# Kernel optimization log

Hardware: AMD Instinct MI355X
Metric: run time of the kernel (lower is better)

## Reference

```python
import jax, jax.numpy as jnp
import numpy as np

BS, NS, NM, NO = 262144, 16, 8, 8

def setup_inputs() -> dict:
    key = jax.random.key(0)
    k = jax.random.split(key, 6)
    z = jax.random.normal(k[0], (BS, NM), dtype=jnp.float32)
    x0 = jax.random.normal(k[1], (BS, NS), dtype=jnp.float32)
    A = jax.random.normal(k[2], (BS, NS, NS), dtype=jnp.float32) * 0.1
    # PSD initial covariance per batch element
    P0 = jnp.einsum('bij,bkj->bik', A, A) + jnp.eye(NS, dtype=jnp.float32)
    phi = jnp.eye(NS, dtype=jnp.float32) + 0.01 * jax.random.normal(k[3], (NS, NS), dtype=jnp.float32)
    H = jax.random.normal(k[4], (NM, NS), dtype=jnp.float32) * 0.3
    C = jax.random.normal(k[5], (NO, NS), dtype=jnp.float32) * 0.3
    Qdiag = jnp.full((NS,), 0.1, dtype=jnp.float32)
    Rdiag = jnp.full((NM,), 0.1, dtype=jnp.float32)
    return {"z": z, "x0": x0, "P0": P0, "phi": phi, "H": H, "C": C,
            "Qdiag": Qdiag, "Rdiag": Rdiag}

def reference(z, x0, P0, phi, H, C, Qdiag, Rdiag):
    # --- predict ---
    x_pred = x0 @ phi.T                                       # [bs, ns]
    P_pred = jnp.einsum('ij,bjk,lk->bil', phi, P0, phi) + jnp.diag(Qdiag)  # phi P phi^T + Q
    # --- innovation ---
    y = z - x_pred @ H.T                                      # [bs, nm]
    S = jnp.einsum('ij,bjk,lk->bil', H, P_pred, H) + jnp.diag(Rdiag)       # H P H^T + R
    Sinv = jnp.linalg.inv(S)                                  # [bs, nm, nm]
    # --- gain and update ---
    K = jnp.einsum('bij,kj,bkl->bil', P_pred, H, Sinv)        # P H^T S^-1 [bs, ns, nm]
    x_new = x_pred + jnp.einsum('bij,bj->bi', K, y)           # [bs, ns]
    P_new = P_pred - jnp.einsum('bij,jk,bkl->bil', K, H, P_pred)  # (I - K H) P
    out = x_new @ C.T                                         # [bs, no]
    return out
```

## Files before the change

kernel.cpp:

```cpp
#include <hip/hip_runtime.h>


#define QFMA(ACC, OFF, A, V) { ACC[(OFF)+0] += (A)*(V).x; ACC[(OFF)+1] += (A)*(V).y; ACC[(OFF)+2] += (A)*(V).z; ACC[(OFF)+3] += (A)*(V).w; }
#define TS 132

__global__ __launch_bounds__(256) void kalman_fused6(
    const float* __restrict__ z,
    const float* __restrict__ x0,
    const float* __restrict__ P0,
    const float* __restrict__ phi,
    const float* __restrict__ Hm,
    const float* __restrict__ Cm,
    const float* __restrict__ Qd,
    const float* __restrict__ Rd,
    float* __restrict__ out,
    int bs)
{
    __shared__ __align__(16) float BnS[8 * 20];
    __shared__ __align__(16) float BTS[16 * 8];
    __shared__ __align__(16) float CpS[8 * 20];
    __shared__ __align__(16) float CQHS[8 * 8];
    __shared__ __align__(16) float ScS[8 * 8];
    __shared__ __align__(16) float x0S[32 * 20];
    __shared__ __align__(16) float Tb[32 * TS];

    const int tid = threadIdx.x;
    const int e = tid >> 3;
    const int i = tid & 7;

    if (tid < 128) {
        const int m = tid >> 4, k = tid & 15;
        float bv = 0.f, cv = 0.f;
#pragma unroll
        for (int j = 0; j < 16; ++j) {
            const float pj = phi[j * 16 + k];
            bv += Hm[m * 16 + j] * pj;
            cv += Cm[m * 16 + j] * pj;
        }
        BnS[m * 20 + k] = bv;
        BTS[k * 8 + m]  = bv;
        CpS[m * 20 + k] = cv;
    }
    if (tid < 64) {
        const int i2 = tid >> 3, j2 = tid & 7;
        float sc = (i2 == j2) ? Rd[i2] : 0.f;
        float cq = 0.f;
#pragma unroll
        for (int k = 0; k < 16; ++k) {
            const float qh = Qd[k] * Hm[j2 * 16 + k];
            sc += Hm[i2 * 16 + k] * qh;
            cq += Cm[i2 * 16 + k] * qh;
        }
        ScS[i2 * 8 + j2]  = sc;
        CQHS[i2 * 8 + j2] = cq;
    }
    __syncthreads();

    const long stride = (long)gridDim.x * 32;
#pragma unroll 1
    for (long b0 = (long)blockIdx.x * 32; b0 < (long)bs; b0 += stride) {
        const long b = b0 + e;
        if (b >= (long)bs) continue;

        float4 Pq[8];
        {
            const float4* P0v = reinterpret_cast<const float4*>(P0 + (size_t)b * 256);
#pragma unroll
            for (int q = 0; q < 4; ++q) {
                Pq[q]     = P0v[i * 4 + q];
                Pq[q + 4] = P0v[(i + 8) * 4 + q];
            }
        }
        const float x0a = x0[b * 16 + i];
        const float x0b = x0[b * 16 + 8 + i];
        float yv = z[b * 8 + i];
        x0S[e * 20 + i]     = x0a;
        x0S[e * 20 + i + 8] = x0b;

        float t0[8], t1[8];
#pragma unroll
        for (int m = 0; m < 8; ++m) { t0[m] = 0.f; t1[m] = 0.f; }
#pragma unroll
        for (int q = 0; q < 4; ++q) {
            const float4 A = Pq[q], B4 = Pq[q + 4];
            const float a[4] = {A.x, A.y, A.z, A.w};
            const float c[4] = {B4.x, B4.y, B4.z, B4.w};
#pragma unroll
            for (int kk = 0; kk < 4; ++kk) {
                const int k = 4 * q + kk;
                const float4 b0v = *reinterpret_cast<const float4*>(&BTS[k * 8 + 0]);
                const float4 b1v = *reinterpret_cast<const float4*>(&BTS[k * 8 + 4]);
                QFMA(t0, 0, a[kk], b0v) QFMA(t0, 4, a[kk], b1v)
                QFMA(t1, 0, c[kk], b0v) QFMA(t1, 4, c[kk], b1v)
            }
        }
        *reinterpret_cast<float4*>(&Tb[e * TS + i * 8 + 0]) = make_float4(t0[0], t0[1], t0[2], t0[3]);
        *reinterpret_cast<float4*>(&Tb[e * TS + i * 8 + 4]) = make_float4(t0[4], t0[5], t0[6], t0[7]);
        *reinterpret_cast<float4*>(&Tb[e * TS + (i + 8) * 8 + 0]) = make_float4(t1[0], t1[1], t1[2], t1[3]);
        *reinterpret_cast<float4*>(&Tb[e * TS + (i + 8) * 8 + 4]) = make_float4(t1[4], t1[5], t1[6], t1[7]);

        float br[16];
#pragma unroll
        for (int q = 0; q < 4; ++q) {
            const float4 A = *reinterpret_cast<const float4*>(&BnS[i * 20 + 4 * q]);
            br[4*q+0] = A.x; br[4*q+1] = A.y; br[4*q+2] = A.z; br[4*q+3] = A.w;
        }

        float s[8];
        {
            const float4 c0 = *reinterpret_cast<const float4*>(&ScS[i * 8 + 0]);
            const float4 c1 = *reinterpret_cast<const float4*>(&ScS[i * 8 + 4]);
            s[0]=c0.x; s[1]=c0.y; s[2]=c0.z; s[3]=c0.w; s[4]=c1.x; s[5]=c1.y; s[6]=c1.z; s[7]=c1.w;
        }
#pragma unroll
        for (int j = 0; j < 16; ++j) {
            const float4 ta = *reinterpret_cast<const float4*>(&Tb[e * TS + j * 8 + 0]);
            const float4 tb = *reinterpret_cast<const float4*>(&Tb[e * TS + j * 8 + 4]);
            const float bij = br[j];
            QFMA(s, 0, bij, ta) QFMA(s, 4, bij, tb)
        }

#pragma unroll
        for (int q = 0; q < 4; ++q) {
            const float4 X = *reinterpret_cast<const float4*>(&x0S[e * 20 + 4 * q]);
            yv -= br[4*q+0]*X.x + br[4*q+1]*X.y + br[4*q+2]*X.z + br[4*q+3]*X.w;
        }

#pragma unroll
        for (int k = 0; k < 7; ++k) {
            float pr[8];
#pragma unroll
            for (int j = k; j < 8; ++j) pr[j] = __shfl(s[j], k, 8);
            const float py = __shfl(yv, k, 8);
            if (i > k) {
                const float f = s[k] / pr[k];
#pragma unroll
                for (int j = k; j < 8; ++j) s[j] -= f * pr[j];
                yv -= f * py;
            }
        }
        float w[8];
#pragma unroll
        for (int k = 7; k >= 0; --k) {
            const float num = __shfl(yv, k, 8);
            const float den = __shfl(s[k], k, 8);
            const float wk = num / den;
            w[k] = wk;
            if (i < k) yv -= s[k] * wk;
        }

        float th0 = 0.f, th1 = 0.f;
#pragma unroll
        for (int m = 0; m < 8; ++m) { th0 += t0[m] * w[m]; th1 += t1[m] * w[m]; }
        const float u0v = x0a + th0;
        const float u1v = x0b + th1;

        float uv[16];
#pragma unroll
        for (int j = 0; j < 8; ++j) {
            uv[j]     = __shfl(u0v, j, 8);
            uv[j + 8] = __shfl(u1v, j, 8);
        }

        float oc = 0.f;
#pragma unroll
        for (int q = 0; q < 4; ++q) {
            const float4 A = *reinterpret_cast<const float4*>(&CpS[i * 20 + 4 * q]);
            oc += A.x*uv[4*q+0] + A.y*uv[4*q+1] + A.z*uv[4*q+2] + A.w*uv[4*q+3];
        }
        {
            const float4 q0 = *reinterpret_cast<const float4*>(&CQHS[i * 8 + 0]);
            const float4 q1 = *reinterpret_cast<const float4*>(&CQHS[i * 8 + 4]);
            oc += q0.x*w[0] + q0.y*w[1] + q0.z*w[2] + q0.w*w[3]
                + q1.x*w[4] + q1.y*w[5] + q1.z*w[6] + q1.w*w[7];
        }
        out[b * 8 + i] = oc;
    }
}

extern "C" void kernel_launch(void* const* d_in, const int* in_sizes, int n_in,
                              void* d_out, int out_size, void* d_ws, size_t ws_size,
                              hipStream_t stream)
{
    const float* z   = (const float*)d_in[0];
    const float* x0  = (const float*)d_in[1];
    const float* P0  = (const float*)d_in[2];
    const float* phi = (const float*)d_in[3];
    const float* H   = (const float*)d_in[4];
    const float* C   = (const float*)d_in[5];
    const float* Qd  = (const float*)d_in[6];
    const float* Rd  = (const float*)d_in[7];
    float* out = (float*)d_out;

    const int bs = in_sizes[0] / 8;
    const int chunks = (bs + 31) / 32;
    const int blocks = (chunks < 1536) ? chunks : 1536;
    hipLaunchKernelGGL(kalman_fused6, dim3(blocks), dim3(256), 0, stream,
                       z, x0, P0, phi, H, C, Qd, Rd, out, bs);
}
```

Baseline: 83.05 us.

## Drop grid-stride loop, prefetch P0 before setup, use redundant per-lane Cholesky solve

Launches one block per 32-element chunk instead of a grid-stride loop. The P0, x0 and z loads are issued before the shared-constant setup and barrier, so global latency overlaps that work. The shuffle-based Gaussian elimination is replaced by a Cholesky factorisation with rsqrt, done redundantly in registers by all 8 lanes after a shared-memory broadcast of S and y. This removes the chain of dependent shuffles, at the cost of more registers and duplicated arithmetic per lane. The final state vector is broadcast through shared memory instead of shuffles.

```diff
diff --git a/kernel.cpp b/kernel.cpp
--- a/kernel.cpp
+++ b/kernel.cpp
@@ -3,8 +3,10 @@
 
 #define QFMA(ACC, OFF, A, V) { ACC[(OFF)+0] += (A)*(V).x; ACC[(OFF)+1] += (A)*(V).y; ACC[(OFF)+2] += (A)*(V).z; ACC[(OFF)+3] += (A)*(V).w; }
 #define TS 132
-
-__global__ __launch_bounds__(256) void kalman_fused6(
+#define XS 28
+#define TRI(a,k) ((a)*((a)+1)/2 + (k))
+
+__global__ __launch_bounds__(256) void kalman_fused7(
     const float* __restrict__ z,
     const float* __restrict__ x0,
     const float* __restrict__ P0,
@@ -21,12 +23,30 @@
     __shared__ __align__(16) float CpS[8 * 20];
     __shared__ __align__(16) float CQHS[8 * 8];
     __shared__ __align__(16) float ScS[8 * 8];
-    __shared__ __align__(16) float x0S[32 * 20];
+    __shared__ __align__(16) float x0S[32 * XS];
     __shared__ __align__(16) float Tb[32 * TS];
 
     const int tid = threadIdx.x;
     const int e = tid >> 3;
     const int i = tid & 7;
+    long b = (long)blockIdx.x * 32 + e;
+    const bool valid = (b < (long)bs);
+    if (!valid) b = (long)bs - 1;
+
+    float4 Pq[8];
+    {
+        const float4* P0v = reinterpret_cast<const float4*>(P0 + (size_t)b * 256);
+#pragma unroll
+        for (int q = 0; q < 4; ++q) {
+            Pq[q]     = P0v[i * 4 + q];
+            Pq[q + 4] = P0v[(i + 8) * 4 + q];
+        }
+    }
+    const float x0a = x0[b * 16 + i];
+    const float x0b = x0[b * 16 + 8 + i];
+    float yv = z[b * 8 + i];
+    x0S[e * XS + i]     = x0a;
+    x0S[e * XS + i + 8] = x0b;
 
     if (tid < 128) {
         const int m = tid >> 4, k = tid & 15;
@@ -56,126 +76,132 @@
     }
     __syncthreads();
 
-    const long stride = (long)gridDim.x * 32;
-#pragma unroll 1
-    for (long b0 = (long)blockIdx.x * 32; b0 < (long)bs; b0 += stride) {
-        const long b = b0 + e;
-        if (b >= (long)bs) continue;
-
-        float4 Pq[8];
-        {
-            const float4* P0v = reinterpret_cast<const float4*>(P0 + (size_t)b * 256);
-#pragma unroll
-            for (int q = 0; q < 4; ++q) {
-                Pq[q]     = P0v[i * 4 + q];
-                Pq[q + 4] = P0v[(i + 8) * 4 + q];
-            }
-        }
-        const float x0a = x0[b * 16 + i];
-        const float x0b = x0[b * 16 + 8 + i];
-        float yv = z[b * 8 + i];
-        x0S[e * 20 + i]     = x0a;
-        x0S[e * 20 + i + 8] = x0b;
-
-        float t0[8], t1[8];
-#pragma unroll
-        for (int m = 0; m < 8; ++m) { t0[m] = 0.f; t1[m] = 0.f; }
-#pragma unroll
-        for (int q = 0; q < 4; ++q) {
-            const float4 A = Pq[q], B4 = Pq[q + 4];
-            const float a[4] = {A.x, A.y, A.z, A.w};
-            const float c[4] = {B4.x, B4.y, B4.z, B4.w};
-#pragma unroll
-            for (int kk = 0; kk < 4; ++kk) {
-                const int k = 4 * q + kk;
-                const float4 b0v = *reinterpret_cast<const float4*>(&BTS[k * 8 + 0]);
-                const float4 b1v = *reinterpret_cast<const float4*>(&BTS[k * 8 + 4]);
-                QFMA(t0, 0, a[kk], b0v) QFMA(t0, 4, a[kk], b1v)
-                QFMA(t1, 0, c[kk], b0v) QFMA(t1, 4, c[kk], b1v)
-            }
-        }
-        *reinterpret_cast<float4*>(&Tb[e * TS + i * 8 + 0]) = make_float4(t0[0], t0[1], t0[2], t0[3]);
-        *reinterpret_cast<float4*>(&Tb[e * TS + i * 8 + 4]) = make_float4(t0[4], t0[5], t0[6], t0[7]);
-        *reinterpret_cast<float4*>(&Tb[e * TS + (i + 8) * 8 + 0]) = make_float4(t1[0], t1[1], t1[2], t1[3]);
-        *reinterpret_cast<float4*>(&Tb[e * TS + (i + 8) * 8 + 4]) = make_float4(t1[4], t1[5], t1[6], t1[7]);
-
-        float br[16];
-#pragma unroll
-        for (int q = 0; q < 4; ++q) {
-            const float4 A = *reinterpret_cast<const float4*>(&BnS[i * 20 + 4 * q]);
-            br[4*q+0] = A.x; br[4*q+1] = A.y; br[4*q+2] = A.z; br[4*q+3] = A.w;
-        }
-
-        float s[8];
-        {
-            const float4 c0 = *reinterpret_cast<const float4*>(&ScS[i * 8 + 0]);
-            const float4 c1 = *reinterpret_cast<const float4*>(&ScS[i * 8 + 4]);
-            s[0]=c0.x; s[1]=c0.y; s[2]=c0.z; s[3]=c0.w; s[4]=c1.x; s[5]=c1.y; s[6]=c1.z; s[7]=c1.w;
-        }
-#pragma unroll
-        for (int j = 0; j < 16; ++j) {
-            const float4 ta = *reinterpret_cast<const float4*>(&Tb[e * TS + j * 8 + 0]);
-            const float4 tb = *reinterpret_cast<const float4*>(&Tb[e * TS + j * 8 + 4]);
-            const float bij = br[j];
-            QFMA(s, 0, bij, ta) QFMA(s, 4, bij, tb)
-        }
-
-#pragma unroll
-        for (int q = 0; q < 4; ++q) {
-            const float4 X = *reinterpret_cast<const float4*>(&x0S[e * 20 + 4 * q]);
-            yv -= br[4*q+0]*X.x + br[4*q+1]*X.y + br[4*q+2]*X.z + br[4*q+3]*X.w;
-        }
-
-#pragma unroll
-        for (int k = 0; k < 7; ++k) {
-            float pr[8];
-#pragma unroll
-            for (int j = k; j < 8; ++j) pr[j] = __shfl(s[j], k, 8);
-            const float py = __shfl(yv, k, 8);
-            if (i > k) {
-                const float f = s[k] / pr[k];
-#pragma unroll
-                for (int j = k; j < 8; ++j) s[j] -= f * pr[j];
-                yv -= f * py;
-            }
-        }
-        float w[8];
-#pragma unroll
-        for (int k = 7; k >= 0; --k) {
-            const float num = __shfl(yv, k, 8);
-            const float den = __shfl(s[k], k, 8);
-            const float wk = num / den;
-            w[k] = wk;
-            if (i < k) yv -= s[k] * wk;
-        }
-
-        float th0 = 0.f, th1 = 0.f;
-#pragma unroll
-        for (int m = 0; m < 8; ++m) { th0 += t0[m] * w[m]; th1 += t1[m] * w[m]; }
-        const float u0v = x0a + th0;
-        const float u1v = x0b + th1;
-
-        float uv[16];
-#pragma unroll
-        for (int j = 0; j < 8; ++j) {
-            uv[j]     = __shfl(u0v, j, 8);
-            uv[j + 8] = __shfl(u1v, j, 8);
-        }
-
-        float oc = 0.f;
-#pragma unroll
-        for (int q = 0; q < 4; ++q) {
-            const float4 A = *reinterpret_cast<const float4*>(&CpS[i * 20 + 4 * q]);
-            oc += A.x*uv[4*q+0] + A.y*uv[4*q+1] + A.z*uv[4*q+2] + A.w*uv[4*q+3];
-        }
-        {
-            const float4 q0 = *reinterpret_cast<const float4*>(&CQHS[i * 8 + 0]);
-            const float4 q1 = *reinterpret_cast<const float4*>(&CQHS[i * 8 + 4]);
-            oc += q0.x*w[0] + q0.y*w[1] + q0.z*w[2] + q0.w*w[3]
-                + q1.x*w[4] + q1.y*w[5] + q1.z*w[6] + q1.w*w[7];
-        }
-        out[b * 8 + i] = oc;
-    }
+    float t0[8], t1[8];
+#pragma unroll
+    for (int m = 0; m < 8; ++m) { t0[m] = 0.f; t1[m] = 0.f; }
+#pragma unroll
+    for (int q = 0; q < 4; ++q) {
+        const float4 A = Pq[q], B4 = Pq[q + 4];
+        const float a[4] = {A.x, A.y, A.z, A.w};
+        const float c[4] = {B4.x, B4.y, B4.z, B4.w};
+#pragma unroll
+        for (int kk = 0; kk < 4; ++kk) {
+            const int k = 4 * q + kk;
+            const float4 b0v = *reinterpret_cast<const float4*>(&BTS[k * 8 + 0]);
+            const float4 b1v = *reinterpret_cast<const float4*>(&BTS[k * 8 + 4]);
+            QFMA(t0, 0, a[kk], b0v) QFMA(t0, 4, a[kk], b1v)
+            QFMA(t1, 0, c[kk], b0v) QFMA(t1, 4, c[kk], b1v)
+        }
+    }
+    *reinterpret_cast<float4*>(&Tb[e * TS + i * 8 + 0]) = make_float4(t0[0], t0[1], t0[2], t0[3]);
+    *reinterpret_cast<float4*>(&Tb[e * TS + i * 8 + 4]) = make_float4(t0[4], t0[5], t0[6], t0[7]);
+    *reinterpret_cast<float4*>(&Tb[e * TS + (i + 8) * 8 + 0]) = make_float4(t1[0], t1[1], t1[2], t1[3]);
+    *reinterpret_cast<float4*>(&Tb[e * TS + (i + 8) * 8 + 4]) = make_float4(t1[4], t1[5], t1[6], t1[7]);
+
+    float br[16];
+#pragma unroll
+    for (int q = 0; q < 4; ++q) {
+        const float4 A = *reinterpret_cast<const float4*>(&BnS[i * 20 + 4 * q]);
+        br[4*q+0] = A.x; br[4*q+1] = A.y; br[4*q+2] = A.z; br[4*q+3] = A.w;
+    }
+
+    float s[8];
+    {
+        const float4 c0 = *reinterpret_cast<const float4*>(&ScS[i * 8 + 0]);
+        const float4 c1 = *reinterpret_cast<const float4*>(&ScS[i * 8 + 4]);
+        s[0]=c0.x; s[1]=c0.y; s[2]=c0.z; s[3]=c0.w; s[4]=c1.x; s[5]=c1.y; s[6]=c1.z; s[7]=c1.w;
+    }
+#pragma unroll
+    for (int j = 0; j < 16; ++j) {
+        const float4 ta = *reinterpret_cast<const float4*>(&Tb[e * TS + j * 8 + 0]);
+        const float4 tb = *reinterpret_cast<const float4*>(&Tb[e * TS + j * 8 + 4]);
+        const float bij = br[j];
+        QFMA(s, 0, bij, ta) QFMA(s, 4, bij, tb)
+    }
+
+#pragma unroll
+    for (int q = 0; q < 4; ++q) {
+        const float4 X = *reinterpret_cast<const float4*>(&x0S[e * XS + 4 * q]);
+        yv -= br[4*q+0]*X.x + br[4*q+1]*X.y + br[4*q+2]*X.z + br[4*q+3]*X.w;
+    }
+
+    *reinterpret_cast<float4*>(&Tb[e * TS + i * 8 + 0]) = make_float4(s[0], s[1], s[2], s[3]);
+    *reinterpret_cast<float4*>(&Tb[e * TS + i * 8 + 4]) = make_float4(s[4], s[5], s[6], s[7]);
+    x0S[e * XS + 16 + i] = yv;
+
+    float L[36];
+#pragma unroll
+    for (int a = 0; a < 8; ++a) {
+        const float4 q0 = *reinterpret_cast<const float4*>(&Tb[e * TS + a * 8 + 0]);
+        L[TRI(a,0)] = q0.x;
+        if (a >= 1) L[TRI(a,1)] = q0.y;
+        if (a >= 2) L[TRI(a,2)] = q0.z;
+        if (a >= 3) L[TRI(a,3)] = q0.w;
+        if (a >= 4) {
+            const float4 q1 = *reinterpret_cast<const float4*>(&Tb[e * TS + a * 8 + 4]);
+            L[TRI(a,4)] = q1.x;
+            if (a >= 5) L[TRI(a,5)] = q1.y;
+            if (a >= 6) L[TRI(a,6)] = q1.z;
+            if (a >= 7) L[TRI(a,7)] = q1.w;
+        }
+    }
+    float yf[8];
+    {
+        const float4 ya = *reinterpret_cast<const float4*>(&x0S[e * XS + 16]);
+        const float4 yb = *reinterpret_cast<const float4*>(&x0S[e * XS + 20]);
+        yf[0]=ya.x; yf[1]=ya.y; yf[2]=ya.z; yf[3]=ya.w;
+        yf[4]=yb.x; yf[5]=yb.y; yf[6]=yb.z; yf[7]=yb.w;
+    }
+
+#pragma unroll
+    for (int k = 0; k < 8; ++k) {
+        const float inv = __builtin_amdgcn_rsqf(L[TRI(k,k)]);
+        L[TRI(k,k)] = inv;
+#pragma unroll
+        for (int a = k + 1; a < 8; ++a) L[TRI(a,k)] *= inv;
+#pragma unroll
+        for (int a = k + 1; a < 8; ++a) {
+#pragma unroll
+            for (int m = k + 1; m <= a; ++m)
+                L[TRI(a,m)] -= L[TRI(a,k)] * L[TRI(m,k)];
+        }
+    }
+#pragma unroll
+    for (int a = 0; a < 8; ++a) {
+        float t = yf[a];
+#pragma unroll
+        for (int j = 0; j < a; ++j) t -= L[TRI(a,j)] * yf[j];
+        yf[a] = t * L[TRI(a,a)];
+    }
+    float w[8];
+#pragma unroll
+    for (int a = 7; a >= 0; --a) {
+        float t = yf[a];
+#pragma unroll
+        for (int j = a + 1; j < 8; ++j) t -= L[TRI(j,a)] * w[j];
+        w[a] = t * L[TRI(a,a)];
+    }
+
+    float th0 = 0.f, th1 = 0.f;
+#pragma unroll
+    for (int m = 0; m < 8; ++m) { th0 += t0[m] * w[m]; th1 += t1[m] * w[m]; }
+    x0S[e * XS + i]     = x0a + th0;
+    x0S[e * XS + i + 8] = x0b + th1;
+
+    float oc = 0.f;
+#pragma unroll
+    for (int q = 0; q < 4; ++q) {
+        const float4 A = *reinterpret_cast<const float4*>(&CpS[i * 20 + 4 * q]);
+        const float4 U = *reinterpret_cast<const float4*>(&x0S[e * XS + 4 * q]);
+        oc += A.x*U.x + A.y*U.y + A.z*U.z + A.w*U.w;
+    }
+    {
+        const float4 q0 = *reinterpret_cast<const float4*>(&CQHS[i * 8 + 0]);
+        const float4 q1 = *reinterpret_cast<const float4*>(&CQHS[i * 8 + 4]);
+        oc += q0.x*w[0] + q0.y*w[1] + q0.z*w[2] + q0.w*w[3]
+            + q1.x*w[4] + q1.y*w[5] + q1.z*w[6] + q1.w*w[7];
+    }
+    if (valid) out[b * 8 + i] = oc;
 }
 
 extern "C" void kernel_launch(void* const* d_in, const int* in_sizes, int n_in,
@@ -193,8 +219,7 @@
     float* out = (float*)d_out;
 
     const int bs = in_sizes[0] / 8;
-    const int chunks = (bs + 31) / 32;
-    const int blocks = (chunks < 1536) ? chunks : 1536;
-    hipLaunchKernelGGL(kalman_fused6, dim3(blocks), dim3(256), 0, stream,
+    const int blocks = (bs + 31) / 32;
+    hipLaunchKernelGGL(kalman_fused7, dim3(blocks), dim3(256), 0, stream,
                        z, x0, P0, phi, H, C, Qd, Rd, out, bs);
 }
```

Measured after the change: 68.11 us. 18.0% less time.
